# Kernel tuning notes

Hardware: AMD Instinct MI355X
Metric: run time of the kernel (lower is better)

Reference implementation:

```python
import jax, jax.numpy as jnp
import numpy as np

KEEPRATE = 0.5


def setup_inputs() -> dict:
    key = jax.random.key(0)
    k1, k2, k3 = jax.random.split(key, 3)
    N, C, T, V, K = 64, 128, 256, 25, 3
    x = jax.random.normal(k1, (N, C, T, V), dtype=jnp.float32)
    A = jax.random.uniform(k2, (N, K, V, V), dtype=jnp.float32)
    p = jax.random.normal(k3, (C * T, 1), dtype=jnp.float32)
    return {"x": x, "A": A, "p": p}


def reference(x, A, p):
    N, C, T, V = x.shape
    Vk = int(KEEPRATE * V)  # number of joints kept
    # [N, V, C*T]
    xr = jnp.transpose(x.reshape(N, C * T, V), (0, 2, 1))
    # l2-normalized projection vector, score per node
    pn = p * jax.lax.rsqrt(jnp.sum(p * p))
    y = xr @ pn                       # [N, V, 1]
    ys = y[..., 0]                    # [N, V]
    idx = jnp.argsort(-ys, axis=-1)[:, :Vk]   # [N, Vk] top-k node indices
    y_hat = jax.nn.sigmoid(jnp.take_along_axis(ys, idx, axis=1))[..., None]  # [N, Vk, 1]
    xg = jnp.take_along_axis(xr, idx[..., None], axis=1) * y_hat             # [N, Vk, C*T]
    # adjacency squaring then row+col gather of kept nodes
    A2 = A @ A                        # [N, K, V, V]

    def _sel(a2, i):                  # a2: [K, V, V], i: [Vk]
        return a2[:, i][:, :, i]      # [K, Vk, Vk]

    A_out = jax.vmap(_sel)(A2, idx)   # [N, K, Vk, Vk]
    x_out = jnp.transpose(xg, (0, 2, 1)).reshape(N, C, T, Vk)
    return x_out, A_out
```

## Files before the change

### kernel.cpp

```cpp
#include <hip/hip_runtime.h>
#include <hip/hip_bf16.h>
#include <math.h>

constexpr int N  = 64;
constexpr int V  = 25;
constexpr int K  = 3;
constexpr int CT = 32768;
constexpr int VK = 12;
constexpr int SPLIT = 32;
constexpr int ROWS  = 256;
constexpr int NF4   = ROWS * V / 4;


__device__ __forceinline__ void gload_lds16(const float* g, float* l) {
    __builtin_amdgcn_global_load_lds(
        (const __attribute__((address_space(1))) void*)g,
        (__attribute__((address_space(3))) void*)l, 16, 0, 0);
}

__device__ __forceinline__ void stage_tile(const float* __restrict__ gsrc, float* lds, int tid) {
    const int wave = tid >> 6, lane = tid & 63;
    for (int b = wave * 64; b < NF4; b += 256) {
        gload_lds16(gsrc + (size_t)(b + lane) * 4, lds + (size_t)b * 4);
    }
}

__global__ __launch_bounds__(256) void k_scores(const float* __restrict__ x, const float* __restrict__ p,
                         float* __restrict__ partial, float* __restrict__ p2partial) {
    const int n = blockIdx.x / SPLIT;
    const int s = blockIdx.x % SPLIT;
    constexpr int CHUNK = CT / SPLIT;
    constexpr int TILES = CHUNK / ROWS;
    const int ct0 = s * CHUNK;
    const float* xn = x + (size_t)n * CT * V;
    const int tid = threadIdx.x;

    __shared__ float lds[ROWS * V];

    float acc[V];
    #pragma unroll
    for (int v = 0; v < V; ++v) acc[v] = 0.f;
    float psq = 0.f;

    for (int tile = 0; tile < TILES; ++tile) {
        const int base_ct = ct0 + tile * ROWS;
        stage_tile(xn + (size_t)base_ct * V, lds, tid);
        asm volatile("s_waitcnt vmcnt(0)" ::: "memory");
        __syncthreads();

        const float pv = p[base_ct + tid];
        psq += pv * pv;
        const float* row = lds + tid * V;
        #pragma unroll
        for (int v = 0; v < V; ++v) acc[v] += row[v] * pv;
        __syncthreads();
    }

    #pragma unroll
    for (int v = 0; v < V; ++v) {
        float a = acc[v];
        #pragma unroll
        for (int off = 32; off > 0; off >>= 1) a += __shfl_down(a, off);
        acc[v] = a;
    }
    #pragma unroll
    for (int off = 32; off > 0; off >>= 1) psq += __shfl_down(psq, off);

    __shared__ float red[4][V];
    __shared__ float redp[4];
    const int lane = tid & 63, wid = tid >> 6;
    if (lane == 0) {
        #pragma unroll
        for (int v = 0; v < V; ++v) red[wid][v] = acc[v];
        redp[wid] = psq;
    }
    __syncthreads();
    if (tid < V) {
        partial[(size_t)blockIdx.x * V + tid] = red[0][tid] + red[1][tid] + red[2][tid] + red[3][tid];
    }
    if (tid == V && n == 0) {
        p2partial[s] = redp[0] + redp[1] + redp[2] + redp[3];
    }
}

__global__ __launch_bounds__(64) void k_topk(const float* __restrict__ partial,
                       const float* __restrict__ p2partial,
                       int* __restrict__ idxbuf, float* __restrict__ yhatbuf) {
    const int n = blockIdx.x;
    __shared__ float ys[V];
    if (threadIdx.x < V) {
        float s = 0.f;
        #pragma unroll
        for (int kk = 0; kk < SPLIT; ++kk) s += partial[((size_t)n * SPLIT + kk) * V + threadIdx.x];
        ys[threadIdx.x] = s;
    }
    __syncthreads();
    if (threadIdx.x < V) {
        const int v = threadIdx.x;
        float s2 = 0.f;
        #pragma unroll
        for (int i = 0; i < SPLIT; ++i) s2 += p2partial[i];
        const float my = ys[v];
        int rank = 0;
        for (int u = 0; u < V; ++u) {
            const float yu = ys[u];
            if (yu > my || (yu == my && u < v)) ++rank;
        }
        if (rank < VK) {
            idxbuf[n * VK + rank]  = v;
            yhatbuf[n * VK + rank] = 1.0f / (1.0f + expf(-my * rsqrtf(s2)));
        }
    }
}

__global__ __launch_bounds__(256) void k_gather_aout(const float* __restrict__ x, const float* __restrict__ A,
                             const int* __restrict__ idxbuf, const float* __restrict__ yhatbuf,
                             float* __restrict__ xout, float* __restrict__ aout) {
    __shared__ float lds[ROWS * V];
    __shared__ int   sidx[VK];
    __shared__ float syh[VK];
    const int tid = threadIdx.x;

    if (blockIdx.x < (unsigned)(N * (CT / ROWS))) {
        const int b  = blockIdx.x;
        const int n  = b >> 7;
        const int r0 = (b & 127) << 8;
        if (tid < VK) {
            sidx[tid] = idxbuf[n * VK + tid];
            syh[tid]  = yhatbuf[n * VK + tid];
        }
        stage_tile(x + ((size_t)n * CT + r0) * V, lds, tid);
        asm volatile("s_waitcnt vmcnt(0)" ::: "memory");
        __syncthreads();

        float4* dst = (float4*)(xout + ((size_t)n * CT + r0) * VK);
        #pragma unroll
        for (int j = 0; j < 3; ++j) {
            const int f   = tid + j * 256;
            const int row = f / 3;
            const int c0  = (f % 3) * 4;
            float4 o;
            o.x = lds[row * V + sidx[c0 + 0]] * syh[c0 + 0];
            o.y = lds[row * V + sidx[c0 + 1]] * syh[c0 + 1];
            o.z = lds[row * V + sidx[c0 + 2]] * syh[c0 + 2];
            o.w = lds[row * V + sidx[c0 + 3]] * syh[c0 + 3];
            dst[f] = o;
        }
    } else {
        const int b2 = blockIdx.x - N * (CT / ROWS);
        const int n  = b2 / K;
        const int k  = b2 % K;
        if (tid < VK) sidx[tid] = idxbuf[n * VK + tid];
        const float* Ak = A + ((size_t)n * K + k) * V * V;
        for (int i = tid; i < V * V; i += 256) lds[i] = Ak[i];
        __syncthreads();
        if (tid < VK * VK) {
            const int a  = tid / VK, bc = tid % VK;
            const int ia = sidx[a], ib = sidx[bc];
            float ssum = 0.f;
            #pragma unroll
            for (int m = 0; m < V; ++m) ssum += lds[ia * V + m] * lds[m * V + ib];
            aout[((size_t)n * K + k) * VK * VK + tid] = ssum;
        }
    }
}

extern "C" void kernel_launch(void* const* d_in, const int* in_sizes, int n_in,
                              void* d_out, int out_size, void* d_ws, size_t ws_size,
                              hipStream_t stream) {
    const float* x = (const float*)d_in[0];
    const float* A = (const float*)d_in[1];
    const float* p = (const float*)d_in[2];

    float* xout = (float*)d_out;
    float* aout = xout + (size_t)N * CT * VK;

    char* ws = (char*)d_ws;
    float* partial   = (float*)(ws);
    float* p2partial = (float*)(ws + 204800);
    float* yhatbuf   = (float*)(ws + 204928);
    int*   idxbuf    = (int*)  (ws + 208000);

    k_scores<<<N * SPLIT, 256, 0, stream>>>(x, p, partial, p2partial);
    k_topk<<<N, 64, 0, stream>>>(partial, p2partial, idxbuf, yhatbuf);
    k_gather_aout<<<N * (CT / ROWS) + N * K, 256, 0, stream>>>(x, A, idxbuf, yhatbuf, xout, aout);
}
```

Baseline: 92.32 us.

## Fuse top-k into gather kernel and switch to per-wave LDS staging without barriers

Removes the separate top-k kernel launch. Every wave of the gather kernel now recomputes the top-k for its batch from a transposed partial-score buffer, using shuffles instead of shared-memory ranking. Tile staging is split so each wave loads exactly the 64 rows it consumes, which removes the block-wide __syncthreads in both the score and gather loops. The cost is redundant top-k work in every wave and extra partial-score reads from global memory.

```diff
diff --git a/kernel.cpp b/kernel.cpp
--- a/kernel.cpp
+++ b/kernel.cpp
@@ -9,7 +9,7 @@
 constexpr int VK = 12;
 constexpr int SPLIT = 32;
 constexpr int ROWS  = 256;
-constexpr int NF4   = ROWS * V / 4;
+constexpr int NBLK_G = N * (CT / ROWS);
 
 
 __device__ __forceinline__ void gload_lds16(const float* g, float* l) {
@@ -18,22 +18,28 @@
         (__attribute__((address_space(3))) void*)l, 16, 0, 0);
 }
 
-__device__ __forceinline__ void stage_tile(const float* __restrict__ gsrc, float* lds, int tid) {
-    const int wave = tid >> 6, lane = tid & 63;
-    for (int b = wave * 64; b < NF4; b += 256) {
-        gload_lds16(gsrc + (size_t)(b + lane) * 4, lds + (size_t)b * 4);
-    }
+__device__ __forceinline__ void stage_wave(const float* __restrict__ gsrc, float* lds,
+                                           int wave, int lane) {
+    const float* gw = gsrc + (size_t)wave * 1600;
+    float* lw = lds + wave * 1600;
+    #pragma unroll
+    for (int i = 0; i < 6; ++i)
+        gload_lds16(gw + (size_t)(i * 64 + lane) * 4, lw + i * 256);
+    if (lane < 16)
+        gload_lds16(gw + (size_t)(384 + lane) * 4, lw + 384 * 4);
 }
 
-__global__ __launch_bounds__(256) void k_scores(const float* __restrict__ x, const float* __restrict__ p,
-                         float* __restrict__ partial, float* __restrict__ p2partial) {
+__global__ __launch_bounds__(256) void k_scores(const float* __restrict__ x,
+                                                const float* __restrict__ p,
+                                                float* __restrict__ partial_t,
+                                                float* __restrict__ p2partial) {
     const int n = blockIdx.x / SPLIT;
     const int s = blockIdx.x % SPLIT;
     constexpr int CHUNK = CT / SPLIT;
     constexpr int TILES = CHUNK / ROWS;
     const int ct0 = s * CHUNK;
     const float* xn = x + (size_t)n * CT * V;
-    const int tid = threadIdx.x;
+    const int tid = threadIdx.x, wave = tid >> 6, lane = tid & 63;
 
     __shared__ float lds[ROWS * V];
 
@@ -44,16 +50,15 @@
 
     for (int tile = 0; tile < TILES; ++tile) {
         const int base_ct = ct0 + tile * ROWS;
-        stage_tile(xn + (size_t)base_ct * V, lds, tid);
+        asm volatile("s_waitcnt lgkmcnt(0)" ::: "memory");
+        stage_wave(xn + (size_t)base_ct * V, lds, wave, lane);
         asm volatile("s_waitcnt vmcnt(0)" ::: "memory");
-        __syncthreads();
 
         const float pv = p[base_ct + tid];
         psq += pv * pv;
         const float* row = lds + tid * V;
         #pragma unroll
         for (int v = 0; v < V; ++v) acc[v] += row[v] * pv;
-        __syncthreads();
     }
 
     #pragma unroll
@@ -68,99 +73,97 @@
 
     __shared__ float red[4][V];
     __shared__ float redp[4];
-    const int lane = tid & 63, wid = tid >> 6;
     if (lane == 0) {
         #pragma unroll
-        for (int v = 0; v < V; ++v) red[wid][v] = acc[v];
-        redp[wid] = psq;
+        for (int v = 0; v < V; ++v) red[wave][v] = acc[v];
+        redp[wave] = psq;
     }
     __syncthreads();
     if (tid < V) {
-        partial[(size_t)blockIdx.x * V + tid] = red[0][tid] + red[1][tid] + red[2][tid] + red[3][tid];
+        partial_t[((size_t)n * V + tid) * SPLIT + s] =
+            red[0][tid] + red[1][tid] + red[2][tid] + red[3][tid];
     }
     if (tid == V && n == 0) {
         p2partial[s] = redp[0] + redp[1] + redp[2] + redp[3];
     }
 }
 
-__global__ __launch_bounds__(64) void k_topk(const float* __restrict__ partial,
-                       const float* __restrict__ p2partial,
-                       int* __restrict__ idxbuf, float* __restrict__ yhatbuf) {
-    const int n = blockIdx.x;
-    __shared__ float ys[V];
-    if (threadIdx.x < V) {
-        float s = 0.f;
+__device__ __forceinline__ void wave_topk(const float* __restrict__ partial_t,
+                                          const float* __restrict__ p2partial,
+                                          int n, int lane, int* swidx, float* swyh) {
+    float s2 = 0.f;
+    #pragma unroll
+    for (int i = 0; i < SPLIT; ++i) s2 += p2partial[i];
+
+    float my = 0.f;
+    if (lane < V) {
+        const float4* pb = (const float4*)(partial_t + ((size_t)n * V + lane) * SPLIT);
         #pragma unroll
-        for (int kk = 0; kk < SPLIT; ++kk) s += partial[((size_t)n * SPLIT + kk) * V + threadIdx.x];
-        ys[threadIdx.x] = s;
+        for (int i = 0; i < SPLIT / 4; ++i) {
+            float4 q = pb[i];
+            my += q.x + q.y + q.z + q.w;
+        }
     }
-    __syncthreads();
-    if (threadIdx.x < V) {
-        const int v = threadIdx.x;
-        float s2 = 0.f;
-        #pragma unroll
-        for (int i = 0; i < SPLIT; ++i) s2 += p2partial[i];
-        const float my = ys[v];
-        int rank = 0;
-        for (int u = 0; u < V; ++u) {
-            const float yu = ys[u];
-            if (yu > my || (yu == my && u < v)) ++rank;
-        }
-        if (rank < VK) {
-            idxbuf[n * VK + rank]  = v;
-            yhatbuf[n * VK + rank] = 1.0f / (1.0f + expf(-my * rsqrtf(s2)));
-        }
+    int rank = 0;
+    #pragma unroll
+    for (int u = 0; u < V; ++u) {
+        const float yu = __shfl(my, u);
+        if (yu > my || (yu == my && u < lane)) ++rank;
+    }
+    if (lane < V && rank < VK) {
+        swidx[rank] = lane;
+        swyh[rank]  = 1.0f / (1.0f + expf(-my * rsqrtf(s2)));
     }
 }
 
-__global__ __launch_bounds__(256) void k_gather_aout(const float* __restrict__ x, const float* __restrict__ A,
-                             const int* __restrict__ idxbuf, const float* __restrict__ yhatbuf,
-                             float* __restrict__ xout, float* __restrict__ aout) {
+__global__ __launch_bounds__(256) void k_gather_aout(const float* __restrict__ x,
+                                                     const float* __restrict__ A,
+                                                     const float* __restrict__ partial_t,
+                                                     const float* __restrict__ p2partial,
+                                                     float* __restrict__ xout,
+                                                     float* __restrict__ aout) {
     __shared__ float lds[ROWS * V];
-    __shared__ int   sidx[VK];
-    __shared__ float syh[VK];
-    const int tid = threadIdx.x;
+    __shared__ int   swidx[4][VK];
+    __shared__ float swyh[4][VK];
+    const int tid = threadIdx.x, wave = tid >> 6, lane = tid & 63;
 
-    if (blockIdx.x < (unsigned)(N * (CT / ROWS))) {
-        const int b  = blockIdx.x;
-        const int n  = b >> 7;
-        const int r0 = (b & 127) << 8;
-        if (tid < VK) {
-            sidx[tid] = idxbuf[n * VK + tid];
-            syh[tid]  = yhatbuf[n * VK + tid];
-        }
-        stage_tile(x + ((size_t)n * CT + r0) * V, lds, tid);
-        asm volatile("s_waitcnt vmcnt(0)" ::: "memory");
-        __syncthreads();
+    if (blockIdx.x < (unsigned)NBLK_G) {
+        const int n  = blockIdx.x >> 7;
+        const int r0 = (blockIdx.x & 127) << 8;
+
+        stage_wave(x + ((size_t)n * CT + r0) * V, lds, wave, lane);
+        wave_topk(partial_t, p2partial, n, lane, swidx[wave], swyh[wave]);
+        asm volatile("s_waitcnt vmcnt(0) lgkmcnt(0)" ::: "memory");
 
         float4* dst = (float4*)(xout + ((size_t)n * CT + r0) * VK);
         #pragma unroll
         for (int j = 0; j < 3; ++j) {
-            const int f   = tid + j * 256;
+            const int f   = 192 * wave + 64 * j + lane;
             const int row = f / 3;
             const int c0  = (f % 3) * 4;
             float4 o;
-            o.x = lds[row * V + sidx[c0 + 0]] * syh[c0 + 0];
-            o.y = lds[row * V + sidx[c0 + 1]] * syh[c0 + 1];
-            o.z = lds[row * V + sidx[c0 + 2]] * syh[c0 + 2];
-            o.w = lds[row * V + sidx[c0 + 3]] * syh[c0 + 3];
+            o.x = lds[row * V + swidx[wave][c0 + 0]] * swyh[wave][c0 + 0];
+            o.y = lds[row * V + swidx[wave][c0 + 1]] * swyh[wave][c0 + 1];
+            o.z = lds[row * V + swidx[wave][c0 + 2]] * swyh[wave][c0 + 2];
+            o.w = lds[row * V + swidx[wave][c0 + 3]] * swyh[wave][c0 + 3];
             dst[f] = o;
         }
     } else {
-        const int b2 = blockIdx.x - N * (CT / ROWS);
+        if (wave != 0) return;
+        const int b2 = blockIdx.x - NBLK_G;
         const int n  = b2 / K;
         const int k  = b2 % K;
-        if (tid < VK) sidx[tid] = idxbuf[n * VK + tid];
+        wave_topk(partial_t, p2partial, n, lane, swidx[0], swyh[0]);
         const float* Ak = A + ((size_t)n * K + k) * V * V;
-        for (int i = tid; i < V * V; i += 256) lds[i] = Ak[i];
-        __syncthreads();
-        if (tid < VK * VK) {
-            const int a  = tid / VK, bc = tid % VK;
-            const int ia = sidx[a], ib = sidx[bc];
+        for (int i = lane; i < V * V; i += 64) lds[i] = Ak[i];
+        asm volatile("s_waitcnt vmcnt(0) lgkmcnt(0)" ::: "memory");
+        for (int o = lane; o < VK * VK; o += 64) {
+            const int a  = o / VK, bc = o % VK;
+            const int ia = swidx[0][a], ib = swidx[0][bc];
             float ssum = 0.f;
             #pragma unroll
             for (int m = 0; m < V; ++m) ssum += lds[ia * V + m] * lds[m * V + ib];
-            aout[((size_t)n * K + k) * VK * VK + tid] = ssum;
+            aout[((size_t)n * K + k) * VK * VK + o] = ssum;
         }
     }
 }
@@ -176,12 +179,9 @@
     float* aout = xout + (size_t)N * CT * VK;
 
     char* ws = (char*)d_ws;
-    float* partial   = (float*)(ws);
+    float* partial_t = (float*)(ws);
     float* p2partial = (float*)(ws + 204800);
-    float* yhatbuf   = (float*)(ws + 204928);
-    int*   idxbuf    = (int*)  (ws + 208000);
 
-    k_scores<<<N * SPLIT, 256, 0, stream>>>(x, p, partial, p2partial);
-    k_topk<<<N, 64, 0, stream>>>(partial, p2partial, idxbuf, yhatbuf);
-    k_gather_aout<<<N * (CT / ROWS) + N * K, 256, 0, stream>>>(x, A, idxbuf, yhatbuf, xout, aout);
+    k_scores<<<N * SPLIT, 256, 0, stream>>>(x, p, partial_t, p2partial);
+    k_gather_aout<<<NBLK_G + N * K, 256, 0, stream>>>(x, A, partial_t, p2partial, xout, aout);
 }
```

Result: slower. 94.20 us (+2.0%).
